# Performance work log

Hardware: AMD Instinct MI355X
Metric: run time of the kernel (lower is better)

Reference implementation:

```python
import jax, jax.numpy as jnp
import numpy as np

B, C, H, W = 16, 512, 64, 64
P = 100        # number of positive proxies
DS = 4         # downsample factor for mask t


def _l2norm(v, axis):
    # torch: v / (sum(v**2, dim, keepdim) + 1e-12) ** 0.5  (eps inside sqrt)
    return v / jnp.sqrt(jnp.sum(v * v, axis=axis, keepdims=True) + 1e-12)


def setup_inputs() -> dict:
    key = jax.random.key(0)
    ks = jax.random.split(key, 5)
    x = jax.random.normal(ks[0], (B, C, H, W), jnp.float32)
    x_gt = jax.random.normal(ks[1], (B, C, H, W), jnp.float32)
    t = jax.random.uniform(ks[2], (B, 1, H * DS, W * DS), jnp.float32)
    has_anomaly = jax.random.uniform(ks[3], (B, 1), jnp.float32)
    # learned params: proxies L2-normalized at init (as in torch __init__)
    pp = jax.random.normal(ks[4], (1, C, P), jnp.float32)
    pp = pp / jnp.sqrt(jnp.sum(pp ** 2, axis=1, keepdims=True) + 1e-12)
    gr = jnp.zeros((1, 1, P), jnp.float32)  # global_representation buffer
    return {"x": x, "x_gt": x_gt, "t": t, "ds": DS, "has_anomaly": has_anomaly,
            "positive_proxies": pp, "global_representation": gr}


def reference(x, x_gt, t, ds, has_anomaly, positive_proxies, global_representation):
    gamma = 1.0 / 0.1
    Bx, Cx, Hx, Wx = x.shape
    HW = Hx * Wx

    # avg_pool2d(t, ds) with kernel=stride=ds, then threshold
    Bt, Ct, Ht, Wt = t.shape
    t_ds_m = t.reshape(Bt, Ct, Ht // ds, ds, Wt // ds, ds).mean(axis=(3, 5))
    t_ds = jnp.where(t_ds_m > 0.02, 1.0, 0.0)
    t_flat_T = t_ds.reshape(Bx, 1, HW).transpose(0, 2, 1)  # (B, HW, 1)

    # L2-normalize features over channel dim
    Fl2 = _l2norm(x.reshape(Bx, Cx, HW), axis=1)           # (B, C, HW)
    Fl2_T = Fl2.transpose(0, 2, 1)                          # (B, HW, C)

    # L2-normalize proxies over channel dim
    pos_prox_l2 = _l2norm(positive_proxies, axis=1)         # (1, C, P)
    Wp = pos_prox_l2[0]                                     # (C, P)

    # cosine similarity + soft assignment
    Fcos_pos = jnp.einsum('bnc,cp->bnp', Fl2_T, Wp)         # (B, HW, P)
    sm = jax.nn.softmax(gamma * Fcos_pos, axis=2)
    Sim_pos = jnp.sum(sm * Fcos_pos, axis=2, keepdims=True) # (B, HW, 1)
    loss_pos = jnp.sum((1.0 - Sim_pos) * (1.0 - t_flat_T)) / (jnp.sum(1.0 - t_flat_T) + 1e-12)

    # proxy_sim_reg_loss: faithful to original (eye(Fcos.shape[0]) = eye(1)
    # broadcasts to an all-zero mask, so this term is identically 0)
    Fcos_pp = jnp.einsum('cp,cq->pq', Wp, Wp)[None]         # (1, P, P)
    reg_mask = 1.0 - jnp.eye(Fcos_pp.shape[0], dtype=x.dtype)  # eye(1) -> zeros after broadcast
    loss_reg = jnp.mean(Fcos_pp * reg_mask)

    # global_rep_reg (proxies detached in original)
    Wp_d = jax.lax.stop_gradient(Wp)
    Fcos_d = jnp.einsum('bnc,cp->bnp', Fl2_T, Wp_d)
    sm_d = jax.nn.softmax(gamma * Fcos_d, axis=2)
    grm = jnp.mean(sm_d, axis=1, keepdims=True)             # (B, 1, P)
    ha = has_anomaly[:, :, None]                            # (B, 1, 1)
    grm = grm * (1.0 - ha)
    grm = jnp.sum(grm, axis=0, keepdims=True) / (jnp.sum(1.0 - ha) + 1e-12)
    loss_global = jnp.mean(jnp.abs(grm - global_representation))

    # proxy_sim_neg_compare: cosine sim between x and x_gt under anomaly mask
    Fl2_gt = _l2norm(x_gt.reshape(Bx, Cx, HW), axis=1)      # (B, C, HW)
    cos_gt = jnp.sum(Fl2 * Fl2_gt, axis=1, keepdims=True)   # (B, 1, HW)
    t_flat = t_flat_T.transpose(0, 2, 1)                    # (B, 1, HW)
    loss_negative = jnp.sum((1.0 - cos_gt) * t_flat) / (jnp.sum(t_flat) + 1e-12)

    return loss_pos + loss_negative + 0.1 * loss_reg + loss_global
```

## Files before the change

### kernel.cpp

```cpp
#include <hip/hip_runtime.h>

#define HW 4096
#define NC 512
#define NP 100
#define NB 16
#define GAMMA 10.0f


__global__ void k_norm_proxies(const float* __restrict__ pp, float* __restrict__ Wp) {
    int p = blockIdx.x;
    int t = threadIdx.x;
    float s = 0.f;
    for (int c = t; c < NC; c += 64) { float v = pp[c * NP + p]; s += v * v; }
    #pragma unroll
    for (int off = 32; off > 0; off >>= 1) s += __shfl_down(s, off);
    s = __shfl(s, 0);
    float inv = 1.0f / sqrtf(s + 1e-12f);
    for (int c = t; c < NC; c += 64) Wp[c * NP + p] = pp[c * NP + p] * inv;
}

__global__ void k_reg2(const float* __restrict__ Wp, float* __restrict__ accums) {
    __shared__ float wsum[8];
    int tid = threadIdx.x;
    const float4* r = reinterpret_cast<const float4*>(Wp + tid * NP);
    float s = 0.f, ss = 0.f;
    #pragma unroll
    for (int j = 0; j < 25; ++j) {
        float4 v = r[j];
        s  += v.x + v.y + v.z + v.w;
        ss += v.x * v.x + v.y * v.y + v.z * v.z + v.w * v.w;
    }
    float contrib = s * s - ss;
    #pragma unroll
    for (int off = 32; off > 0; off >>= 1) contrib += __shfl_xor(contrib, off);
    if ((tid & 63) == 0) wsum[tid >> 6] = contrib;
    __syncthreads();
    if (tid == 0) {
        float tot = 0.f;
        #pragma unroll
        for (int i = 0; i < 8; ++i) tot += wsum[i];
        accums[3] = tot;
    }
}

__device__ __forceinline__ void proc8(const float (&xr)[8], const float (&gr)[8],
                                      const float* wbase, float (&acc)[NP],
                                      float& sxx, float& sgg, float& sxg) {
    #pragma unroll
    for (int i = 0; i < 8; ++i) {
        float xv = xr[i], gv = gr[i];
        sxx = fmaf(xv, xv, sxx);
        sgg = fmaf(gv, gv, sgg);
        sxg = fmaf(xv, gv, sxg);
        const float* wrow = wbase + i * NP;
        #pragma unroll
        for (int q = 0; q < 25; ++q) {
            float4 w4 = *reinterpret_cast<const float4*>(wrow + 4 * q);
            acc[4*q+0] = fmaf(xv, w4.x, acc[4*q+0]);
            acc[4*q+1] = fmaf(xv, w4.y, acc[4*q+1]);
            acc[4*q+2] = fmaf(xv, w4.z, acc[4*q+2]);
            acc[4*q+3] = fmaf(xv, w4.w, acc[4*q+3]);
        }
    }
}

__global__ __launch_bounds__(256, 2)
void k_main(
        const float* __restrict__ x, const float* __restrict__ xgt,
        const float* __restrict__ t, const float* __restrict__ ha,
        const float* __restrict__ Wp, float* __restrict__ accums) {
    __shared__ __align__(16) float wlds[12928];
    __shared__ float scx[128 * 4];
    __shared__ float grmLDS[NP];
    __shared__ float scal[3];

    int tid  = threadIdx.x;
    int half = tid >> 7;
    int hidx = tid & 127;
    int point = blockIdx.x * 128 + hidx;
    int b = point >> 12;
    int n = point & (HW - 1);

    if (tid < NP) grmLDS[tid] = 0.f;
    if (tid < 3)  scal[tid]  = 0.f;

    float tf = 0.f;
    if (half == 0) {
        int h = n >> 6, w = n & 63;
        const float* tb = t + (size_t)b * (256 * 256) + (h * 4) * 256 + w * 4;
        float ts = 0.f;
        #pragma unroll
        for (int i = 0; i < 4; ++i) {
            float4 v = *reinterpret_cast<const float4*>(tb + i * 256);
            ts += v.x + v.y + v.z + v.w;
        }
        tf = (ts * (1.0f / 16.0f) > 0.02f) ? 1.0f : 0.0f;
    }

    const float* xp = x   + (size_t)b * (NC * HW) + (size_t)(half * 256) * HW + n;
    const float* gp = xgt + (size_t)b * (NC * HW) + (size_t)(half * 256) * HW + n;

    float acc[NP];
    #pragma unroll
    for (int p = 0; p < NP; ++p) acc[p] = 0.f;
    float sxx = 0.f, sgg = 0.f, sxg = 0.f;

    float xa[8], ga[8], xb[8], gb[8];
    #pragma unroll
    for (int i = 0; i < 8; ++i) { xa[i] = xp[(size_t)i * HW]; ga[i] = gp[(size_t)i * HW]; }

    float* wbuf = wlds + half * 6400;
    float4* wl4 = reinterpret_cast<float4*>(wbuf);

    for (int seg = 0; seg < 4; ++seg) {
        __syncthreads();
        const float4* ws4 = reinterpret_cast<const float4*>(Wp + (half * 256 + seg * 64) * NP);
        #pragma unroll 4
        for (int j = 0; j < 12; ++j) wl4[hidx + j * 128] = ws4[hidx + j * 128];
        if (hidx < 64) wl4[1536 + hidx] = ws4[1536 + hidx];
        __syncthreads();

        #pragma unroll
        for (int cc = 0; cc < 8; cc += 2) {
            int k = seg * 8 + cc;
            {
                const float* xc = xp + (size_t)(k + 1) * 8 * HW;
                const float* gc = gp + (size_t)(k + 1) * 8 * HW;
                #pragma unroll
                for (int i = 0; i < 8; ++i) { xb[i] = xc[(size_t)i * HW]; gb[i] = gc[(size_t)i * HW]; }
            }
            proc8(xa, ga, wbuf + (cc * 8) * NP, acc, sxx, sgg, sxg);
            if (k + 2 < 32) {
                const float* xc = xp + (size_t)(k + 2) * 8 * HW;
                const float* gc = gp + (size_t)(k + 2) * 8 * HW;
                #pragma unroll
                for (int i = 0; i < 8; ++i) { xa[i] = xc[(size_t)i * HW]; ga[i] = gc[(size_t)i * HW]; }
            }
            proc8(xb, gb, wbuf + ((cc + 1) * 8) * NP, acc, sxx, sgg, sxg);
        }
    }

    __syncthreads();
    if (half == 1) {
        scx[hidx * 4 + 0] = sxx;
        scx[hidx * 4 + 1] = sgg;
        scx[hidx * 4 + 2] = sxg;
        float* dst = wlds + hidx * 101;
        #pragma unroll
        for (int p = 0; p < NP; ++p) dst[p] = acc[p];
    }
    __syncthreads();

    if (half == 0) {
        sxx += scx[hidx * 4 + 0];
        sgg += scx[hidx * 4 + 1];
        sxg += scx[hidx * 4 + 2];
        const float* src = wlds + hidx * 101;
        #pragma unroll
        for (int p = 0; p < NP; ++p) acc[p] += src[p];

        float invx = 1.0f / sqrtf(sxx + 1e-12f);
        float m = -1e30f;
        #pragma unroll
        for (int p = 0; p < NP; ++p) { acc[p] *= invx; m = fmaxf(m, acc[p]); }
        float s = 0.f, sf = 0.f;
        #pragma unroll
        for (int p = 0; p < NP; ++p) {
            float ev = __expf(GAMMA * (acc[p] - m));
            s += ev; sf = fmaf(ev, acc[p], sf);
            acc[p] = ev;
        }
        float Sim   = sf / s;
        float invg  = 1.0f / sqrtf(sgg + 1e-12f);
        float cosgt = sxg * invx * invg;

        int lane = tid & 63;
        float v0 = (1.0f - Sim)   * (1.0f - tf);
        float v1 = (1.0f - cosgt) * tf;
        float v2 = tf;
        #pragma unroll
        for (int off = 32; off > 0; off >>= 1) {
            v0 += __shfl_xor(v0, off);
            v1 += __shfl_xor(v1, off);
            v2 += __shfl_xor(v2, off);
        }
        if (lane == 0) {
            atomicAdd(&scal[0], v0);
            atomicAdd(&scal[1], v1);
            atomicAdd(&scal[2], v2);
        }
        float winv = (1.0f - ha[b]) / s;
        #pragma unroll
        for (int p = 0; p < NP; ++p) {
            float g = acc[p] * winv;
            #pragma unroll
            for (int off = 32; off > 0; off >>= 1) g += __shfl_xor(g, off);
            if (lane == 0) atomicAdd(&grmLDS[p], g);
        }
    }
    __syncthreads();
    if (tid < NP) atomicAdd(&accums[8 + tid], grmLDS[tid]);
    if (tid < 3)  atomicAdd(&accums[tid], scal[tid]);
}

__global__ void k_final(const float* __restrict__ accums, const float* __restrict__ ha,
                        const float* __restrict__ gr, float* __restrict__ out) {
    __shared__ float red;
    int t = threadIdx.x;
    if (t == 0) red = 0.f;
    __syncthreads();
    float S = 0.f;
    #pragma unroll
    for (int b2 = 0; b2 < NB; ++b2) S += 1.0f - ha[b2];
    float contrib = 0.f;
    if (t < NP) {
        float g = accums[8 + t] / (4096.0f * (S + 1e-12f));
        contrib = fabsf(g - gr[t]);
    }
    atomicAdd(&red, contrib);
    __syncthreads();
    if (t == 0) {
        float num_pos = accums[0], num_neg = accums[1], sum_t = accums[2], reg = accums[3];
        float den_pos = (float)(NB * HW) - sum_t;
        float loss_pos = num_pos / (den_pos + 1e-12f);
        float loss_neg = num_neg / (sum_t + 1e-12f);
        float loss_reg = reg / (float)(NP * NP);
        float loss_glob = red / (float)NP;
        out[0] = loss_pos + loss_neg + 0.1f * loss_reg + loss_glob;
    }
}

extern "C" void kernel_launch(void* const* d_in, const int* in_sizes, int n_in,
                              void* d_out, int out_size, void* d_ws, size_t ws_size,
                              hipStream_t stream) {
    const float* x   = (const float*)d_in[0];
    const float* xgt = (const float*)d_in[1];
    const float* t   = (const float*)d_in[2];
    const float* ha  = (const float*)d_in[4];
    const float* pp  = (const float*)d_in[5];
    const float* gr  = (const float*)d_in[6];
    float* out = (float*)d_out;

    float* Wp     = (float*)d_ws;
    float* accums = Wp + 51200;

    hipMemsetAsync(accums, 0, 128 * sizeof(float), stream);
    k_norm_proxies<<<100, 64, 0, stream>>>(pp, Wp);
    k_reg2<<<1, 512, 0, stream>>>(Wp, accums);
    k_main<<<512, 256, 0, stream>>>(x, xgt, t, ha, Wp, accums);
    k_final<<<1, 128, 0, stream>>>(accums, ha, gr, out);
}
```

Measured before the change: 6.121 ms.

## Split proxy dimension across thread halves instead of channel dimension

Each half of the block now computes 50 of the 100 proxy similarities over all 512 channels, rather than all 100 proxies over half the channels. This halves the accumulator registers per thread, which allows raising launch bounds to 4 blocks per CU and shrinks the shared-memory weight buffer. The cost is that both halves read the full x and x_gt columns, doubling global load requests, though these may hit in cache. The softmax is assembled by combining each half's results through shared memory.

```diff
diff --git a/kernel.cpp b/kernel.cpp
--- a/kernel.cpp
+++ b/kernel.cpp
@@ -3,6 +3,7 @@
 #define HW 4096
 #define NC 512
 #define NP 100
+#define NPH 50
 #define NB 16
 #define GAMMA 10.0f
 
@@ -44,7 +45,7 @@
 }
 
 __device__ __forceinline__ void proc8(const float (&xr)[8], const float (&gr)[8],
-                                      const float* wbase, float (&acc)[NP],
+                                      const float* wbase, float (&acc)[NPH],
                                       float& sxx, float& sgg, float& sxg) {
     #pragma unroll
     for (int i = 0; i < 8; ++i) {
@@ -52,30 +53,27 @@
         sxx = fmaf(xv, xv, sxx);
         sgg = fmaf(gv, gv, sgg);
         sxg = fmaf(xv, gv, sxg);
-        const float* wrow = wbase + i * NP;
+        const float2* wrow = reinterpret_cast<const float2*>(wbase + i * NP);
         #pragma unroll
         for (int q = 0; q < 25; ++q) {
-            float4 w4 = *reinterpret_cast<const float4*>(wrow + 4 * q);
-            acc[4*q+0] = fmaf(xv, w4.x, acc[4*q+0]);
-            acc[4*q+1] = fmaf(xv, w4.y, acc[4*q+1]);
-            acc[4*q+2] = fmaf(xv, w4.z, acc[4*q+2]);
-            acc[4*q+3] = fmaf(xv, w4.w, acc[4*q+3]);
-        }
-    }
-}
-
-__global__ __launch_bounds__(256, 2)
+            float2 w2 = wrow[q];
+            acc[2*q+0] = fmaf(xv, w2.x, acc[2*q+0]);
+            acc[2*q+1] = fmaf(xv, w2.y, acc[2*q+1]);
+        }
+    }
+}
+
+__global__ __launch_bounds__(256, 4)
 void k_main(
         const float* __restrict__ x, const float* __restrict__ xgt,
         const float* __restrict__ t, const float* __restrict__ ha,
         const float* __restrict__ Wp, float* __restrict__ accums) {
-    __shared__ __align__(16) float wlds[12928];
-    __shared__ float scx[128 * 4];
+    __shared__ __align__(16) float wlds[6528];
     __shared__ float grmLDS[NP];
     __shared__ float scal[3];
 
     int tid  = threadIdx.x;
-    int half = tid >> 7;
+    int pi   = tid >> 7;
     int hidx = tid & 127;
     int point = blockIdx.x * 128 + hidx;
     int b = point >> 12;
@@ -85,7 +83,7 @@
     if (tid < 3)  scal[tid]  = 0.f;
 
     float tf = 0.f;
-    if (half == 0) {
+    if (pi == 0) {
         int h = n >> 6, w = n & 63;
         const float* tb = t + (size_t)b * (256 * 256) + (h * 4) * 256 + w * 4;
         float ts = 0.f;
@@ -97,27 +95,26 @@
         tf = (ts * (1.0f / 16.0f) > 0.02f) ? 1.0f : 0.0f;
     }
 
-    const float* xp = x   + (size_t)b * (NC * HW) + (size_t)(half * 256) * HW + n;
-    const float* gp = xgt + (size_t)b * (NC * HW) + (size_t)(half * 256) * HW + n;
-
-    float acc[NP];
-    #pragma unroll
-    for (int p = 0; p < NP; ++p) acc[p] = 0.f;
+    const float* xp = x   + (size_t)b * (NC * HW) + n;
+    const float* gp = xgt + (size_t)b * (NC * HW) + n;
+
+    float acc[NPH];
+    #pragma unroll
+    for (int p = 0; p < NPH; ++p) acc[p] = 0.f;
     float sxx = 0.f, sgg = 0.f, sxg = 0.f;
 
     float xa[8], ga[8], xb[8], gb[8];
     #pragma unroll
     for (int i = 0; i < 8; ++i) { xa[i] = xp[(size_t)i * HW]; ga[i] = gp[(size_t)i * HW]; }
 
-    float* wbuf = wlds + half * 6400;
-    float4* wl4 = reinterpret_cast<float4*>(wbuf);
-
-    for (int seg = 0; seg < 4; ++seg) {
+    float4* wl4 = reinterpret_cast<float4*>(wlds);
+
+    for (int seg = 0; seg < 8; ++seg) {
         __syncthreads();
-        const float4* ws4 = reinterpret_cast<const float4*>(Wp + (half * 256 + seg * 64) * NP);
-        #pragma unroll 4
-        for (int j = 0; j < 12; ++j) wl4[hidx + j * 128] = ws4[hidx + j * 128];
-        if (hidx < 64) wl4[1536 + hidx] = ws4[1536 + hidx];
+        const float4* ws4 = reinterpret_cast<const float4*>(Wp + seg * 64 * NP);
+        #pragma unroll
+        for (int j = 0; j < 6; ++j) wl4[tid + j * 256] = ws4[tid + j * 256];
+        if (tid < 64) wl4[1536 + tid] = ws4[1536 + tid];
         __syncthreads();
 
         #pragma unroll
@@ -129,46 +126,48 @@
                 #pragma unroll
                 for (int i = 0; i < 8; ++i) { xb[i] = xc[(size_t)i * HW]; gb[i] = gc[(size_t)i * HW]; }
             }
-            proc8(xa, ga, wbuf + (cc * 8) * NP, acc, sxx, sgg, sxg);
-            if (k + 2 < 32) {
+            proc8(xa, ga, wlds + (cc * 8) * NP + pi * NPH, acc, sxx, sgg, sxg);
+            if (k + 2 < 64) {
                 const float* xc = xp + (size_t)(k + 2) * 8 * HW;
                 const float* gc = gp + (size_t)(k + 2) * 8 * HW;
                 #pragma unroll
                 for (int i = 0; i < 8; ++i) { xa[i] = xc[(size_t)i * HW]; ga[i] = gc[(size_t)i * HW]; }
             }
-            proc8(xb, gb, wbuf + ((cc + 1) * 8) * NP, acc, sxx, sgg, sxg);
-        }
-    }
-
-    __syncthreads();
-    if (half == 1) {
-        scx[hidx * 4 + 0] = sxx;
-        scx[hidx * 4 + 1] = sgg;
-        scx[hidx * 4 + 2] = sxg;
-        float* dst = wlds + hidx * 101;
-        #pragma unroll
-        for (int p = 0; p < NP; ++p) dst[p] = acc[p];
-    }
-    __syncthreads();
-
-    if (half == 0) {
-        sxx += scx[hidx * 4 + 0];
-        sgg += scx[hidx * 4 + 1];
-        sxg += scx[hidx * 4 + 2];
-        const float* src = wlds + hidx * 101;
-        #pragma unroll
-        for (int p = 0; p < NP; ++p) acc[p] += src[p];
-
+            proc8(xb, gb, wlds + ((cc + 1) * 8) * NP + pi * NPH, acc, sxx, sgg, sxg);
+        }
+    }
+
+    __syncthreads();
+    if (pi == 1) {
+        float* dst = wlds + hidx * 51;
+        #pragma unroll
+        for (int j = 0; j < NPH; ++j) dst[j] = acc[j];
+    }
+    __syncthreads();
+
+    if (pi == 0) {
         float invx = 1.0f / sqrtf(sxx + 1e-12f);
+        float* src = wlds + hidx * 51;
+
         float m = -1e30f;
         #pragma unroll
-        for (int p = 0; p < NP; ++p) { acc[p] *= invx; m = fmaxf(m, acc[p]); }
+        for (int p = 0; p < NPH; ++p) { acc[p] *= invx; m = fmaxf(m, acc[p]); }
+        #pragma unroll
+        for (int p = 0; p < NPH; ++p) m = fmaxf(m, src[p] * invx);
+
         float s = 0.f, sf = 0.f;
         #pragma unroll
-        for (int p = 0; p < NP; ++p) {
+        for (int p = 0; p < NPH; ++p) {
             float ev = __expf(GAMMA * (acc[p] - m));
             s += ev; sf = fmaf(ev, acc[p], sf);
             acc[p] = ev;
+        }
+        #pragma unroll
+        for (int p = 0; p < NPH; ++p) {
+            float v  = src[p] * invx;
+            float ev = __expf(GAMMA * (v - m));
+            s += ev; sf = fmaf(ev, v, sf);
+            src[p] = ev;
         }
         float Sim   = sf / s;
         float invg  = 1.0f / sqrtf(sgg + 1e-12f);
@@ -191,11 +190,18 @@
         }
         float winv = (1.0f - ha[b]) / s;
         #pragma unroll
-        for (int p = 0; p < NP; ++p) {
+        for (int p = 0; p < NPH; ++p) {
             float g = acc[p] * winv;
             #pragma unroll
             for (int off = 32; off > 0; off >>= 1) g += __shfl_xor(g, off);
             if (lane == 0) atomicAdd(&grmLDS[p], g);
+        }
+        #pragma unroll
+        for (int p = 0; p < NPH; ++p) {
+            float g = src[p] * winv;
+            #pragma unroll
+            for (int off = 32; off > 0; off >>= 1) g += __shfl_xor(g, off);
+            if (lane == 0) atomicAdd(&grmLDS[NPH + p], g);
         }
     }
     __syncthreads();
```

Result: slower. 6.286 ms (+2.7%).
